# Kernel optimization log

Measured on AMD Instinct MI355X. Metric: run time of the kernel, lower is better.

Reference implementation:

```python
import jax, jax.numpy as jnp
import numpy as np

N_QUBITS = 8
DEPTH = 2
INPUT_DIM = 128
HIDDEN = 128
SEQ = 128
BATCH = 512
DIM = 2 ** N_QUBITS

# Z expectation signs: wire 0 is the most-significant qubit of the state index.
_bits = (np.arange(DIM)[None, :] >> (N_QUBITS - 1 - np.arange(N_QUBITS)[:, None])) & 1
Z_SIGNS = jnp.asarray(1.0 - 2.0 * _bits, dtype=jnp.float32)  # [n_wires, DIM]


def _apply_1q(state, mat, wire):
    """Apply a 2x2 gate on `wire`. mat: [2,2] or batched [bsz,2,2]."""
    bsz = state.shape[0]
    st = state.reshape(bsz, 2 ** wire, 2, -1)
    if mat.ndim == 3:
        out = jnp.einsum('bij,bxjy->bxiy', mat, st)
    else:
        out = jnp.einsum('ij,bxjy->bxiy', mat, st)
    return out.reshape(bsz, DIM)


def _rx_mat(theta):  # theta: [bsz] -> [bsz,2,2] complex
    c = jnp.cos(theta * 0.5).astype(jnp.complex64)
    s = ((-1j) * jnp.sin(theta * 0.5)).astype(jnp.complex64)
    return jnp.stack([jnp.stack([c, s], -1), jnp.stack([s, c], -1)], -2)


def _ry_mat(theta):  # scalar theta -> [2,2] complex
    c = jnp.cos(theta * 0.5)
    s = jnp.sin(theta * 0.5)
    return jnp.stack([jnp.stack([c, -s]), jnp.stack([s, c])]).astype(jnp.complex64)


def _cnot_adj(state, wire):
    """CNOT control=wire, target=wire+1 (adjacent wires)."""
    bsz = state.shape[0]
    st = state.reshape(bsz, 2 ** wire, 4, -1)
    st = st[:, :, jnp.array([0, 1, 3, 2]), :]  # |10>-><|11| swap
    return st.reshape(bsz, DIM)


def _qgate(q_in, params):
    """Variational circuit: RX encoding (first N_QUBITS features of q_in),
    DEPTH x (RY layer + CNOT chain), measure Z on each wire."""
    bsz = q_in.shape[0]
    state = jnp.zeros((bsz, DIM), jnp.complex64).at[:, 0].set(1.0)
    for w in range(N_QUBITS):
        state = _apply_1q(state, _rx_mat(q_in[:, w]), w)
    for d in range(DEPTH):
        for w in range(N_QUBITS):
            state = _apply_1q(state, _ry_mat(params[d, w]), w)
        for w in range(N_QUBITS - 1):
            state = _cnot_adj(state, w)
    probs = state.real ** 2 + state.imag ** 2  # [bsz, DIM]
    return probs @ Z_SIGNS.T  # [bsz, n_wires]


def setup_inputs() -> dict:
    key = jax.random.key(0)
    ks = jax.random.split(key, 16)
    d_in = INPUT_DIM + HIDDEN
    inv = 1.0 / jnp.sqrt(jnp.float32(d_in))
    invq = 1.0 / jnp.sqrt(jnp.float32(N_QUBITS))
    return {
        'inputs': jax.random.normal(ks[0], (SEQ, BATCH, INPUT_DIM), jnp.float32),
        'Wq': jax.random.normal(ks[1], (4 * N_QUBITS, d_in), jnp.float32) * inv,
        'bq': jnp.zeros((4 * N_QUBITS,), jnp.float32),
        'pf': jax.random.normal(ks[2], (DEPTH, N_QUBITS), jnp.float32),
        'pi': jax.random.normal(ks[3], (DEPTH, N_QUBITS), jnp.float32),
        'pg': jax.random.normal(ks[4], (DEPTH, N_QUBITS), jnp.float32),
        'po': jax.random.normal(ks[5], (DEPTH, N_QUBITS), jnp.float32),
        'Wf': jax.random.normal(ks[6], (HIDDEN, N_QUBITS), jnp.float32) * invq,
        'bf': jnp.zeros((HIDDEN,), jnp.float32),
        'Wi': jax.random.normal(ks[7], (HIDDEN, N_QUBITS), jnp.float32) * invq,
        'bi': jnp.zeros((HIDDEN,), jnp.float32),
        'Wg': jax.random.normal(ks[8], (HIDDEN, N_QUBITS), jnp.float32) * invq,
        'bg': jnp.zeros((HIDDEN,), jnp.float32),
        'Wo': jax.random.normal(ks[9], (HIDDEN, N_QUBITS), jnp.float32) * invq,
        'bo': jnp.zeros((HIDDEN,), jnp.float32),
    }


def reference(inputs, Wq, bq, pf, pi, pg, po, Wf, bf, Wi, bi, Wg, bg, Wo, bo):
    bsz = inputs.shape[1]
    h0 = jnp.zeros((bsz, HIDDEN), jnp.float32)
    c0 = jnp.zeros((bsz, HIDDEN), jnp.float32)

    def step(carry, x):
        hx, cx = carry
        combined = jnp.concatenate([x, hx], axis=1)
        q_in = combined @ Wq.T + bq  # [bsz, 4*n_qubits]; only first n_qubits used per gate
        f = jax.nn.sigmoid(_qgate(q_in, pf) @ Wf.T + bf)
        i = jax.nn.sigmoid(_qgate(q_in, pi) @ Wi.T + bi)
        g = jnp.tanh(_qgate(q_in, pg) @ Wg.T + bg)
        o = jax.nn.sigmoid(_qgate(q_in, po) @ Wo.T + bo)
        cx_new = f * cx + i * g
        hx_new = o * jnp.tanh(cx_new)
        return (hx_new, cx_new), hx_new

    (hx, cx), outputs = jax.lax.scan(step, (h0, c0), inputs)
    return outputs, hx, cx
```

## Files before the change

kernel.cpp:

```cpp
#include <hip/hip_runtime.h>

#define SEQ 128
#define BATCH 512
#define IN_DIM 128
#define HID 128

typedef float vf2 __attribute__((ext_vector_type(2)));

#define LOG2E 1.4426950408889634f
#define INV2PI 0.15915494309189535f

__device__ __forceinline__ float rcp_f(float x) { return __builtin_amdgcn_rcpf(x); }
__device__ __forceinline__ float exp2_f(float x) { float r; asm("v_exp_f32 %0, %1" : "=v"(r) : "v"(x)); return r; }
__device__ __forceinline__ float sin2pi_f(float x) { float r; asm("v_sin_f32 %0, %1" : "=v"(r) : "v"(x)); return r; }
__device__ __forceinline__ float cos2pi_f(float x) { float r; asm("v_cos_f32 %0, %1" : "=v"(r) : "v"(x)); return r; }
__device__ __forceinline__ float tanh_f(float x) {
  return 1.0f - 2.0f * rcp_f(exp2_f(x * 2.885390082f) + 1.0f);
}

template <int CTRL>
__device__ __forceinline__ float dpp_add(float s) {
  return s + __int_as_float(__builtin_amdgcn_mov_dpp(__float_as_int(s), CTRL, 0xF, 0xF, true));
}
__device__ __forceinline__ float rdlane(float v, int src) {
  return __int_as_float(__builtin_amdgcn_readlane(__float_as_int(v), src));
}

__device__ __forceinline__ void quarter_bcast(float x, float& r0, float& r1, float& r2, float& r3) {
  unsigned xu = __float_as_uint(x);
  auto pr = __builtin_amdgcn_permlane32_swap(xu, xu, false, false);
#if __has_builtin(__builtin_amdgcn_permlane16_swap)
  auto lo = __builtin_amdgcn_permlane16_swap(pr[0], pr[0], false, false);
  auto hi = __builtin_amdgcn_permlane16_swap(pr[1], pr[1], false, false);
  r0 = __uint_as_float(lo[0]); r1 = __uint_as_float(lo[1]);
  r2 = __uint_as_float(hi[0]); r3 = __uint_as_float(hi[1]);
#else
  unsigned s0 = (unsigned)__builtin_amdgcn_ds_swizzle((int)pr[0], 0x401F);
  unsigned s1 = (unsigned)__builtin_amdgcn_ds_swizzle((int)pr[1], 0x401F);
  const bool qo = (threadIdx.x >> 4) & 1;
  r0 = __uint_as_float(qo ? s0 : pr[0]);
  r1 = __uint_as_float(qo ? pr[0] : s0);
  r2 = __uint_as_float(qo ? s1 : pr[1]);
  r3 = __uint_as_float(qo ? pr[1] : s1);
#endif
}

__global__ __launch_bounds__(64) void qlstm_kernel(
    const float* __restrict__ X, const float* __restrict__ Wq, const float* __restrict__ bq,
    const float* __restrict__ pf, const float* __restrict__ pi_, const float* __restrict__ pg,
    const float* __restrict__ po, const float* __restrict__ Wf, const float* __restrict__ bf,
    const float* __restrict__ Wi, const float* __restrict__ bi, const float* __restrict__ Wg,
    const float* __restrict__ bg, const float* __restrict__ Wo, const float* __restrict__ bo,
    float* __restrict__ out)
{
  __shared__ __align__(16) float h_sh[HID];

  const int lane = threadIdx.x;
  const int r = lane >> 3, c = lane & 7;
  const int g = lane >> 4, p = lane & 15;
  const int b = blockIdx.x;
  const int D0 = 8 * p + 2 * g;
  const bool gsel1 = (g & 1);
  const bool gsel2 = (g >= 2);

  const float* gW = (g == 0) ? Wf : (g == 1) ? Wi : (g == 2) ? Wg : Wo;
  const float* gB = (g == 0) ? bf : (g == 1) ? bi : (g == 2) ? bg : bo;
  const float* gP = (g == 0) ? pf : (g == 1) ? pi_ : (g == 2) ? pg : po;

  vf2 wx[8], wh[8];
  {
    const vf2* pxw = (const vf2*)(Wq + r * 256 + 16 * c);
    const vf2* phw = (const vf2*)(Wq + r * 256 + 128 + 16 * c);
#pragma unroll
    for (int j = 0; j < 8; ++j) { wx[j] = pxw[j] * INV2PI; wh[j] = phw[j] * INV2PI; }
  }
  const float bqv = bq[r] * INV2PI;

  const float amul = (g == 2) ? 2.0f : 1.0f;
  const float oadd = (g == 2) ? -1.0f : 0.0f;
  const float ksc  = -amul * LOG2E;

  vf2 wg2[8][4];
#pragma unroll
  for (int w = 0; w < 8; ++w)
#pragma unroll
    for (int j = 0; j < 4; ++j) {
      wg2[w][j].x = gW[(8 * p + 2 * j)     * 8 + w] * ksc;
      wg2[w][j].y = gW[(8 * p + 2 * j + 1) * 8 + w] * ksc;
    }
  vf2 bias2[4];
#pragma unroll
  for (int j = 0; j < 4; ++j) {
    bias2[j].x = gB[8 * p + 2 * j]     * ksc;
    bias2[j].y = gB[8 * p + 2 * j + 1] * ksc;
  }
  vf2 cbsb[8]; float C1[8], S1[8];
#pragma unroll
  for (int w = 0; w < 8; ++w) {
    float th0 = gP[w], th1 = gP[8 + w];
    cbsb[w].x = cosf(th0); cbsb[w].y = sinf(th0);
    C1[w] = cosf(th1); S1[w] = sinf(th1);
  }

  vf2 c2; c2.x = 0.f; c2.y = 0.f;
  vf2 h2v; h2v.x = 0.f; h2v.y = 0.f;
  float4 hh0 = {0,0,0,0}, hh1 = {0,0,0,0}, hh2 = {0,0,0,0}, hh3 = {0,0,0,0};

  const float* xg = X + (size_t)b * IN_DIM + 16 * c;
  float* outp = out + (size_t)b * HID + D0;
  const float4* hp4 = (const float4*)(h_sh + 16 * c);

  float xp_cur;
  {
    const float4* x0_ = (const float4*)xg;
    float4 a0 = x0_[0], a1 = x0_[1], a2 = x0_[2], a3 = x0_[3];
    vf2 t0 = wx[0] * (vf2){a0.x, a0.y} + wx[1] * (vf2){a0.z, a0.w};
    vf2 t1 = wx[2] * (vf2){a1.x, a1.y} + wx[3] * (vf2){a1.z, a1.w};
    vf2 t2 = wx[4] * (vf2){a2.x, a2.y} + wx[5] * (vf2){a2.z, a2.w};
    vf2 t3 = wx[6] * (vf2){a3.x, a3.y} + wx[7] * (vf2){a3.z, a3.w};
    vf2 ax = (t0 + t1) + (t2 + t3);
    xp_cur = ax.x + ax.y;
  }

#pragma unroll 1
  for (int t = 0; t < SEQ; ++t) {
    float4 xl0, xl1, xl2, xl3;
    {
      const int tn = (t + 1 < SEQ) ? t + 1 : SEQ - 1;
      const float4* xn_ = (const float4*)(xg + (size_t)tn * (BATCH * IN_DIM));
      xl0 = xn_[0]; xl1 = xn_[1]; xl2 = xn_[2]; xl3 = xn_[3];
    }

    float zz;
    {
      vf2 t0 = wh[0] * (vf2){hh0.x, hh0.y} + wh[1] * (vf2){hh0.z, hh0.w};
      vf2 t1 = wh[2] * (vf2){hh1.x, hh1.y} + wh[3] * (vf2){hh1.z, hh1.w};
      vf2 t2 = wh[4] * (vf2){hh2.x, hh2.y} + wh[5] * (vf2){hh2.z, hh2.w};
      vf2 t3 = wh[6] * (vf2){hh3.x, hh3.y} + wh[7] * (vf2){hh3.z, hh3.w};
      vf2 aq = ((t0 + t1) + (t2 + t3)) + (vf2){xp_cur, 0.0f};
      float s_ = aq.x + aq.y;
      s_ = dpp_add<0xB1>(s_); s_ = dpp_add<0x4E>(s_); s_ = dpp_add<0x141>(s_);
      zz = s_ + bqv;
    }
    float szv = sin2pi_f(zz), czv = cos2pi_f(zz);

    float cqs[8], sqs[8];
#pragma unroll
    for (int w = 0; w < 8; ++w) { cqs[w] = rdlane(czv, 8 * w); sqs[w] = rdlane(szv, 8 * w); }

    vf2 acc0 = bias2[0], acc1 = bias2[1], acc2 = bias2[2], acc3 = bias2[3];
    float u_, d_, P_, R_;
    {
      vf2 KA0 = cbsb[0] * cqs[0];
      u_ = C1[0]; d_ = C1[0] * KA0.x;
      P_ = -S1[0] * KA0.y; R_ = -S1[0] * sqs[0];
    }
#pragma unroll
    for (int w = 1; w < 8; ++w) {
      vf2 KA = cbsb[w] * cqs[w];
      float K_ = KA.x, A2_ = KA.y, B2_ = sqs[w];
      float Md = fmaf(A2_, P_, d_);
      float MP = fmaf(A2_, d_, P_);
      float Mu = fmaf(K_, u_, -(B2_ * R_));
      float MR = fmaf(B2_, u_, K_ * R_);
      acc0 += Md * wg2[w - 1][0]; acc1 += Md * wg2[w - 1][1];
      acc2 += Md * wg2[w - 1][2]; acc3 += Md * wg2[w - 1][3];
      u_ = C1[w] * Md; d_ = C1[w] * Mu;
      P_ = -S1[w] * MP; R_ = -S1[w] * MR;
    }
    float ev7_ = d_ + P_;
    acc0 += ev7_ * wg2[7][0]; acc1 += ev7_ * wg2[7][1];
    acc2 += ev7_ * wg2[7][2]; acc3 += ev7_ * wg2[7][3];

    float av_[8] = {acc0.x, acc0.y, acc1.x, acc1.y, acc2.x, acc2.y, acc3.x, acc3.y};
    float o8[8];
#pragma unroll
    for (int k = 0; k < 8; ++k) {
      float e_ = exp2_f(av_[k]);
      o8[k] = fmaf(rcp_f(1.0f + e_), amul, oadd);
    }

    float rE[4][4], rO[4][4];
#pragma unroll
    for (int j = 0; j < 4; ++j) {
      quarter_bcast(o8[2 * j],     rE[j][0], rE[j][1], rE[j][2], rE[j][3]);
      quarter_bcast(o8[2 * j + 1], rO[j][0], rO[j][1], rO[j][2], rO[j][3]);
    }
    vf2 fv, iv, gv, ov;
    {
      float lo, hi;
#define SEL4(A0, A1, A2, A3, DST) \
      lo = gsel1 ? (A1) : (A0); hi = gsel1 ? (A3) : (A2); DST = gsel2 ? hi : lo;
      SEL4(rE[0][0], rE[1][0], rE[2][0], rE[3][0], fv.x)
      SEL4(rO[0][0], rO[1][0], rO[2][0], rO[3][0], fv.y)
      SEL4(rE[0][1], rE[1][1], rE[2][1], rE[3][1], iv.x)
      SEL4(rO[0][1], rO[1][1], rO[2][1], rO[3][1], iv.y)
      SEL4(rE[0][2], rE[1][2], rE[2][2], rE[3][2], gv.x)
      SEL4(rO[0][2], rO[1][2], rO[2][2], rO[3][2], gv.y)
      SEL4(rE[0][3], rE[1][3], rE[2][3], rE[3][3], ov.x)
      SEL4(rO[0][3], rO[1][3], rO[2][3], rO[3][3], ov.y)
#undef SEL4
    }

    c2 = fv * c2 + iv * gv;
    h2v.x = ov.x * tanh_f(c2.x);
    h2v.y = ov.y * tanh_f(c2.y);

    *(vf2*)(h_sh + D0) = h2v;
    hh0 = hp4[0]; hh1 = hp4[1]; hh2 = hp4[2]; hh3 = hp4[3];

    {
      vf2 t0 = wx[0] * (vf2){xl0.x, xl0.y} + wx[1] * (vf2){xl0.z, xl0.w};
      vf2 t1 = wx[2] * (vf2){xl1.x, xl1.y} + wx[3] * (vf2){xl1.z, xl1.w};
      vf2 t2 = wx[4] * (vf2){xl2.x, xl2.y} + wx[5] * (vf2){xl2.z, xl2.w};
      vf2 t3 = wx[6] * (vf2){xl3.x, xl3.y} + wx[7] * (vf2){xl3.z, xl3.w};
      vf2 axn = (t0 + t1) + (t2 + t3);
      xp_cur = axn.x + axn.y;
    }
    *(vf2*)(outp + (size_t)t * (BATCH * HID)) = h2v;
  }

  {
    size_t base = (size_t)SEQ * BATCH * HID;
    *(vf2*)(out + base + (size_t)b * HID + D0) = h2v;
    *(vf2*)(out + base + (size_t)BATCH * HID + (size_t)b * HID + D0) = c2;
  }
}

extern "C" void kernel_launch(void* const* d_in, const int* in_sizes, int n_in,
                              void* d_out, int out_size, void* d_ws, size_t ws_size,
                              hipStream_t stream) {
  (void)in_sizes; (void)n_in; (void)out_size; (void)d_ws; (void)ws_size;
  const float* X   = (const float*)d_in[0];
  const float* Wq  = (const float*)d_in[1];
  const float* bq  = (const float*)d_in[2];
  const float* pf  = (const float*)d_in[3];
  const float* pi_ = (const float*)d_in[4];
  const float* pg  = (const float*)d_in[5];
  const float* po  = (const float*)d_in[6];
  const float* Wf  = (const float*)d_in[7];
  const float* bf  = (const float*)d_in[8];
  const float* Wi  = (const float*)d_in[9];
  const float* bi  = (const float*)d_in[10];
  const float* Wg  = (const float*)d_in[11];
  const float* bg  = (const float*)d_in[12];
  const float* Wo  = (const float*)d_in[13];
  const float* bo  = (const float*)d_in[14];
  float* out = (float*)d_out;

  qlstm_kernel<<<BATCH, 64, 0, stream>>>(X, Wq, bq, pf, pi_, pg, po,
                                         Wf, bf, Wi, bi, Wg, bg, Wo, bo, out);
}
```

Before: 214.6 us.

## Remap gate lanes to cut cross-lane exchange and pad shared h buffer

Lanes are reassigned so the four gates for a given hidden unit sit in lanes differing by bits 3 and 5. The gate-weight columns are pre-permuted by g^m, so each lane needs only one DPP row-shift and one permlane32 swap instead of the full quarter broadcast of eight values. The shared hidden buffer is padded (80-byte stride per 16 floats) to avoid LDS bank conflicts on the float4 reads. The next-step X prefetch is moved later so it issues after the sin/cos. The aim is to shorten the per-timestep serial critical path, at the cost of more intricate lane-index logic.

```diff
diff --git a/kernel.cpp b/kernel.cpp
--- a/kernel.cpp
+++ b/kernel.cpp
@@ -22,27 +22,17 @@
 __device__ __forceinline__ float dpp_add(float s) {
   return s + __int_as_float(__builtin_amdgcn_mov_dpp(__float_as_int(s), CTRL, 0xF, 0xF, true));
 }
+template <int CTRL>
+__device__ __forceinline__ float dpp_mov(float s) {
+  return __int_as_float(__builtin_amdgcn_mov_dpp(__float_as_int(s), CTRL, 0xF, 0xF, true));
+}
 __device__ __forceinline__ float rdlane(float v, int src) {
   return __int_as_float(__builtin_amdgcn_readlane(__float_as_int(v), src));
 }
-
-__device__ __forceinline__ void quarter_bcast(float x, float& r0, float& r1, float& r2, float& r3) {
+__device__ __forceinline__ float xor32_f(float x, bool hi) {
   unsigned xu = __float_as_uint(x);
   auto pr = __builtin_amdgcn_permlane32_swap(xu, xu, false, false);
-#if __has_builtin(__builtin_amdgcn_permlane16_swap)
-  auto lo = __builtin_amdgcn_permlane16_swap(pr[0], pr[0], false, false);
-  auto hi = __builtin_amdgcn_permlane16_swap(pr[1], pr[1], false, false);
-  r0 = __uint_as_float(lo[0]); r1 = __uint_as_float(lo[1]);
-  r2 = __uint_as_float(hi[0]); r3 = __uint_as_float(hi[1]);
-#else
-  unsigned s0 = (unsigned)__builtin_amdgcn_ds_swizzle((int)pr[0], 0x401F);
-  unsigned s1 = (unsigned)__builtin_amdgcn_ds_swizzle((int)pr[1], 0x401F);
-  const bool qo = (threadIdx.x >> 4) & 1;
-  r0 = __uint_as_float(qo ? s0 : pr[0]);
-  r1 = __uint_as_float(qo ? pr[0] : s0);
-  r2 = __uint_as_float(qo ? s1 : pr[1]);
-  r3 = __uint_as_float(qo ? pr[1] : s1);
-#endif
+  return __uint_as_float(hi ? pr[0] : pr[1]);
 }
 
 __global__ __launch_bounds__(64) void qlstm_kernel(
@@ -53,15 +43,16 @@
     const float* __restrict__ bg, const float* __restrict__ Wo, const float* __restrict__ bo,
     float* __restrict__ out)
 {
-  __shared__ __align__(16) float h_sh[HID];
+  __shared__ __align__(16) float h_sw[160];
 
   const int lane = threadIdx.x;
   const int r = lane >> 3, c = lane & 7;
-  const int g = lane >> 4, p = lane & 15;
+  const bool b3v = (lane >> 3) & 1;
+  const bool b5v = (lane >> 5) & 1;
+  const int g = (b5v ? 2 : 0) + (b3v ? 1 : 0);
+  const int p = ((lane >> 4) & 1) * 8 + (lane & 7);
+  const int D0 = 8 * p + 2 * g;
   const int b = blockIdx.x;
-  const int D0 = 8 * p + 2 * g;
-  const bool gsel1 = (g & 1);
-  const bool gsel2 = (g >= 2);
 
   const float* gW = (g == 0) ? Wf : (g == 1) ? Wi : (g == 2) ? Wg : Wo;
   const float* gB = (g == 0) ? bf : (g == 1) ? bi : (g == 2) ? bg : bo;
@@ -81,18 +72,17 @@
   const float ksc  = -amul * LOG2E;
 
   vf2 wg2[8][4];
-#pragma unroll
-  for (int w = 0; w < 8; ++w)
-#pragma unroll
-    for (int j = 0; j < 4; ++j) {
-      wg2[w][j].x = gW[(8 * p + 2 * j)     * 8 + w] * ksc;
-      wg2[w][j].y = gW[(8 * p + 2 * j + 1) * 8 + w] * ksc;
-    }
   vf2 bias2[4];
 #pragma unroll
-  for (int j = 0; j < 4; ++j) {
-    bias2[j].x = gB[8 * p + 2 * j]     * ksc;
-    bias2[j].y = gB[8 * p + 2 * j + 1] * ksc;
+  for (int m = 0; m < 4; ++m) {
+    const int dm = 8 * p + 2 * (g ^ m);
+#pragma unroll
+    for (int w = 0; w < 8; ++w) {
+      wg2[w][m].x = gW[dm * 8 + w] * ksc;
+      wg2[w][m].y = gW[(dm + 1) * 8 + w] * ksc;
+    }
+    bias2[m].x = gB[dm] * ksc;
+    bias2[m].y = gB[dm + 1] * ksc;
   }
   vf2 cbsb[8]; float C1[8], S1[8];
 #pragma unroll
@@ -108,7 +98,8 @@
 
   const float* xg = X + (size_t)b * IN_DIM + 16 * c;
   float* outp = out + (size_t)b * HID + D0;
-  const float4* hp4 = (const float4*)(h_sh + 16 * c);
+  char* hb    = (char*)h_sw + 80 * c;
+  char* hwp   = (char*)h_sw + 80 * (D0 >> 4) + 4 * (D0 & 15);
 
   float xp_cur;
   {
@@ -124,13 +115,6 @@
 
 #pragma unroll 1
   for (int t = 0; t < SEQ; ++t) {
-    float4 xl0, xl1, xl2, xl3;
-    {
-      const int tn = (t + 1 < SEQ) ? t + 1 : SEQ - 1;
-      const float4* xn_ = (const float4*)(xg + (size_t)tn * (BATCH * IN_DIM));
-      xl0 = xn_[0]; xl1 = xn_[1]; xl2 = xn_[2]; xl3 = xn_[3];
-    }
-
     float zz;
     {
       vf2 t0 = wh[0] * (vf2){hh0.x, hh0.y} + wh[1] * (vf2){hh0.z, hh0.w};
@@ -143,6 +127,13 @@
       zz = s_ + bqv;
     }
     float szv = sin2pi_f(zz), czv = cos2pi_f(zz);
+
+    float4 xl0, xl1, xl2, xl3;
+    {
+      const int tn = (t + 1 < SEQ) ? t + 1 : SEQ - 1;
+      const float4* xn_ = (const float4*)(xg + (size_t)tn * (BATCH * IN_DIM));
+      xl0 = xn_[0]; xl1 = xn_[1]; xl2 = xn_[2]; xl3 = xn_[3];
+    }
 
     float cqs[8], sqs[8];
 #pragma unroll
@@ -172,42 +163,45 @@
     acc0 += ev7_ * wg2[7][0]; acc1 += ev7_ * wg2[7][1];
     acc2 += ev7_ * wg2[7][2]; acc3 += ev7_ * wg2[7][3];
 
-    float av_[8] = {acc0.x, acc0.y, acc1.x, acc1.y, acc2.x, acc2.y, acc3.x, acc3.y};
-    float o8[8];
-#pragma unroll
-    for (int k = 0; k < 8; ++k) {
-      float e_ = exp2_f(av_[k]);
-      o8[k] = fmaf(rcp_f(1.0f + e_), amul, oadd);
-    }
-
-    float rE[4][4], rO[4][4];
-#pragma unroll
-    for (int j = 0; j < 4; ++j) {
-      quarter_bcast(o8[2 * j],     rE[j][0], rE[j][1], rE[j][2], rE[j][3]);
-      quarter_bcast(o8[2 * j + 1], rO[j][0], rO[j][1], rO[j][2], rO[j][3]);
+    vf2 pm0, pm1, pm2, pm3;
+    pm0.x = fmaf(rcp_f(1.0f + exp2_f(acc0.x)), amul, oadd);
+    pm0.y = fmaf(rcp_f(1.0f + exp2_f(acc0.y)), amul, oadd);
+    pm1.x = fmaf(rcp_f(1.0f + exp2_f(acc1.x)), amul, oadd);
+    pm1.y = fmaf(rcp_f(1.0f + exp2_f(acc1.y)), amul, oadd);
+    pm2.x = fmaf(rcp_f(1.0f + exp2_f(acc2.x)), amul, oadd);
+    pm2.y = fmaf(rcp_f(1.0f + exp2_f(acc2.y)), amul, oadd);
+    pm3.x = fmaf(rcp_f(1.0f + exp2_f(acc3.x)), amul, oadd);
+    pm3.y = fmaf(rcp_f(1.0f + exp2_f(acc3.y)), amul, oadd);
+
+    vf2 r1, r2, r3;
+    r1.x = dpp_mov<0x128>(pm1.x);
+    r1.y = dpp_mov<0x128>(pm1.y);
+    r2.x = xor32_f(pm2.x, b5v);
+    r2.y = xor32_f(pm2.y, b5v);
+    {
+      float t0 = dpp_mov<0x128>(pm3.x);
+      float t1 = dpp_mov<0x128>(pm3.y);
+      r3.x = xor32_f(t0, b5v);
+      r3.y = xor32_f(t1, b5v);
     }
     vf2 fv, iv, gv, ov;
     {
-      float lo, hi;
-#define SEL4(A0, A1, A2, A3, DST) \
-      lo = gsel1 ? (A1) : (A0); hi = gsel1 ? (A3) : (A2); DST = gsel2 ? hi : lo;
-      SEL4(rE[0][0], rE[1][0], rE[2][0], rE[3][0], fv.x)
-      SEL4(rO[0][0], rO[1][0], rO[2][0], rO[3][0], fv.y)
-      SEL4(rE[0][1], rE[1][1], rE[2][1], rE[3][1], iv.x)
-      SEL4(rO[0][1], rO[1][1], rO[2][1], rO[3][1], iv.y)
-      SEL4(rE[0][2], rE[1][2], rE[2][2], rE[3][2], gv.x)
-      SEL4(rO[0][2], rO[1][2], rO[2][2], rO[3][2], gv.y)
-      SEL4(rE[0][3], rE[1][3], rE[2][3], rE[3][3], ov.x)
-      SEL4(rO[0][3], rO[1][3], rO[2][3], rO[3][3], ov.y)
-#undef SEL4
+      vf2 lo, hi;
+      lo = b3v ? r1 : pm0;  hi = b3v ? r3 : r2;  fv = b5v ? hi : lo;
+      lo = b3v ? pm0 : r1;  hi = b3v ? r2 : r3;  iv = b5v ? hi : lo;
+      lo = b3v ? r3 : r2;   hi = b3v ? r1 : pm0; gv = b5v ? hi : lo;
+      lo = b3v ? r2 : r3;   hi = b3v ? pm0 : r1; ov = b5v ? hi : lo;
     }
 
     c2 = fv * c2 + iv * gv;
     h2v.x = ov.x * tanh_f(c2.x);
     h2v.y = ov.y * tanh_f(c2.y);
 
-    *(vf2*)(h_sh + D0) = h2v;
-    hh0 = hp4[0]; hh1 = hp4[1]; hh2 = hp4[2]; hh3 = hp4[3];
+    *(vf2*)hwp = h2v;
+    hh0 = *(const float4*)(hb);
+    hh1 = *(const float4*)(hb + 16);
+    hh2 = *(const float4*)(hb + 32);
+    hh3 = *(const float4*)(hb + 48);
 
     {
       vf2 t0 = wx[0] * (vf2){xl0.x, xl0.y} + wx[1] * (vf2){xl0.z, xl0.w};
```

Measured after the change: 201.6 us. 1.06x faster.
